# Kernel optimization log

Hardware: AMD Instinct MI355X
Metric: run time of the kernel (lower is better)

The kernel has to match this reference:

```python
import jax, jax.numpy as jnp
import numpy as np

L = 3          # layers
D = 256        # hidden_dim
H = 4          # heads
F = 1024       # ffn_size
IMG = (64, 32) # img_dim
S = IMG[0] * IMG[1]
DK = D // H    # key/query head dim
V = 2 * D      # double_v_dim value dim
DV = V // H    # value head dim
B = 2


def _rel_pos():
    # rotary angles, repeated pairwise as in get_rel_pos
    angle = 1.0 / (10000.0 ** jnp.linspace(0.0, 1.0, DK // 2))
    angle = jnp.repeat(angle, 2)                                  # [DK]
    idx = jnp.arange(S, dtype=jnp.float32)
    sin = jnp.sin(idx[:, None] * angle[None, :])                  # [S, DK]
    cos = jnp.cos(idx[:, None] * angle[None, :])
    # per-head causal decay mask, row-normalized by sqrt(rowsum)
    decay = jnp.log(1.0 - 2.0 ** (-5.0 - jnp.arange(H, dtype=jnp.float32)))  # [H]
    diff = idx[:, None] - idx[None, :]                            # [S, S]
    mask = jnp.where(diff >= 0, jnp.exp(diff[None, :, :] * decay[:, None, None]), 0.0)
    mask = mask / jnp.sqrt(mask.sum(-1, keepdims=True))           # [H, S, S]
    return sin, cos, mask


def _theta_shift(x, sin, cos):
    # x: [B, H, S, DK]; rotate-every-two rotary embedding
    x1, x2 = x[..., ::2], x[..., 1::2]
    rot = jnp.stack([-x2, x1], axis=-1).reshape(x.shape)
    return x * cos + rot * sin


def _ln(x, w, b, eps=1e-5):
    mu = x.mean(-1, keepdims=True)
    var = ((x - mu) ** 2).mean(-1, keepdims=True)
    return (x - mu) / jnp.sqrt(var + eps) * w + b


def _retention(x, sin, cos, mask, Wq, Wk, Wv, Wg, Wo):
    b, s, _ = x.shape
    q = (x @ Wq).reshape(b, s, H, DK).transpose(0, 2, 1, 3)
    k = (x @ Wk).reshape(b, s, H, DK).transpose(0, 2, 1, 3) * (DK ** -0.5)
    v = (x @ Wv).reshape(b, s, H, DV).transpose(0, 2, 1, 3)
    g = x @ Wg                                                    # [b, s, V]
    qr = _theta_shift(q, sin, cos)
    kr = _theta_shift(k, sin, cos)
    qk = jnp.einsum('bhsd,bhtd->bhst', qr, kr) * mask[None]
    denom = jnp.clip(jnp.abs(qk).sum(-1, keepdims=True), 1.0, None)
    qk = qk / jax.lax.stop_gradient(denom)
    o = jnp.einsum('bhst,bhtv->bhsv', qk, v)                      # [b, H, s, DV]
    o = o * jax.lax.rsqrt((o ** 2).mean(-1, keepdims=True) + 1e-6)  # per-head RMSNorm
    o = o.transpose(0, 2, 1, 3).reshape(b, s, V)
    o = (g * jax.nn.sigmoid(g)) * o                               # swish gate
    return o @ Wo


def setup_inputs():
    key = jax.random.key(0)
    ks = jax.random.split(key, 16)
    sc = 0.02
    return {
        'x': jax.random.normal(ks[0], (B, S, D), jnp.float32),
        'Wq': jax.random.normal(ks[1], (L, D, D), jnp.float32) * sc,
        'Wk': jax.random.normal(ks[2], (L, D, D), jnp.float32) * sc,
        'Wv': jax.random.normal(ks[3], (L, D, V), jnp.float32) * sc,
        'Wg': jax.random.normal(ks[4], (L, D, V), jnp.float32) * sc,
        'Wo': jax.random.normal(ks[5], (L, V, D), jnp.float32) * sc,
        'ln1_w': jnp.ones((L, D), jnp.float32),
        'ln1_b': jnp.zeros((L, D), jnp.float32),
        'ln2_w': jnp.ones((L, D), jnp.float32),
        'ln2_b': jnp.zeros((L, D), jnp.float32),
        'W1': jax.random.normal(ks[6], (L, D, F), jnp.float32) * sc,
        'b1': jnp.zeros((L, F), jnp.float32),
        'W2': jax.random.normal(ks[7], (L, F, D), jnp.float32) * sc,
        'b2': jnp.zeros((L, D), jnp.float32),
    }


def reference(x, Wq, Wk, Wv, Wg, Wo, ln1_w, ln1_b, ln2_w, ln2_b, W1, b1, W2, b2):
    sin, cos, mask = _rel_pos()
    for i in range(L):
        y = _retention(_ln(x, ln1_w[i], ln1_b[i]), sin, cos, mask,
                       Wq[i], Wk[i], Wv[i], Wg[i], Wo[i]) + x
        h = _ln(y, ln2_w[i], ln2_b[i])
        x = (jax.nn.gelu(h @ W1[i] + b1[i], approximate=False) @ W2[i] + b2[i]) + y
    return x.reshape(x.shape[0], IMG[0], IMG[1], D)
```

## Files before the change

### kernel.cpp

```cpp
#include <hip/hip_runtime.h>
#include <hip/hip_bf16.h>
#include <cstddef>
#include <cmath>
#include <algorithm>

#define SEQ 2048
#define DMODEL 256
#define NHEAD 4
#define DK 64
#define VDIM 512
#define DV 128
#define NB 2
#define FDIM 1024
#define NROWS (NB*SEQ)
#define QKVGN 1536
#define NSLOT 288

typedef unsigned short u16;
typedef __attribute__((ext_vector_type(8))) short short8;
typedef __attribute__((ext_vector_type(4))) short short4v;
typedef __attribute__((ext_vector_type(4))) float f32x4;

static __device__ __forceinline__ u16 f2b(float f) {
    union { float f; unsigned u; } c; c.f = f;
    unsigned r = c.u + 0x7fffu + ((c.u >> 16) & 1u);
    return (u16)(r >> 16);
}
static __device__ __forceinline__ float b2f(u16 u) {
    union { unsigned u; float f; } c; c.u = ((unsigned)u) << 16; return c.f;
}

static __device__ __forceinline__ f32x4 mfma16_bf16(short4v a, short4v b, f32x4 c) {
    return __builtin_amdgcn_mfma_f32_16x16x16bf16_1k(a, b, c, 0, 0, 0);
}

static __device__ __forceinline__ short4v pack_bf16x4(float a0, float a1, float a2, float a3) {
    union { short4v v; unsigned u[2]; } z;
    union { __hip_bfloat162 h; unsigned u; } p0, p1;
    p0.h = __float22bfloat162_rn(make_float2(a0, a1));
    p1.h = __float22bfloat162_rn(make_float2(a2, a3));
    z.u[0] = p0.u; z.u[1] = p1.u;
    return z.v;
}

#define GLOAD_LDS16(GP, LP) \
    __builtin_amdgcn_global_load_lds((const __attribute__((address_space(1))) void*)(GP), \
                                     (__attribute__((address_space(3))) void*)(LP), 16, 0, 0)

__global__ void tables_kernel(float* __restrict__ sint, float* __restrict__ cost)
{
    int idx = blockIdx.x * 256 + threadIdx.x;
    if (idx >= SEQ * DK) return;
    int s = idx >> 6, d = idx & 63;
    int j = d >> 1;
    float a = powf(10000.f, -(float)j / 31.f);
    float arg = (float)s * a;
    sint[idx] = sinf(arg);
    cost[idx] = cosf(arg);
}

__global__ __launch_bounds__(256) void wconv_kernel(const float* __restrict__ in,
                                                    u16* __restrict__ out, int K, int N,
                                                    size_t in_lstride, size_t out_lstride)
{
    __shared__ float tile[32][33];
    int n0 = blockIdx.x * 32, k0 = blockIdx.y * 32;
    const float* inz = in + (size_t)blockIdx.z * in_lstride;
    u16* outz = out + (size_t)blockIdx.z * out_lstride;
    int tx = threadIdx.x, ty = threadIdx.y;
    #pragma unroll
    for (int r = 0; r < 4; ++r) {
        int kr = ty + r * 8;
        tile[kr][tx] = inz[(size_t)(k0 + kr) * N + n0 + tx];
    }
    __syncthreads();
    #pragma unroll
    for (int r = 0; r < 4; ++r) {
        int nr = ty + r * 8;
        outz[(size_t)(n0 + nr) * K + k0 + tx] = f2b(tile[tx][nr]);
    }
}

__global__ __launch_bounds__(256) void ln_kernel(const float* __restrict__ x,
                                                 const float* __restrict__ w,
                                                 const float* __restrict__ b,
                                                 u16* __restrict__ o)
{
    int row = blockIdx.x;
    int t = threadIdx.x;
    float v = x[(size_t)row * DMODEL + t];
    __shared__ float red[256];
    red[t] = v; __syncthreads();
    for (int st = 128; st > 0; st >>= 1) { if (t < st) red[t] += red[t + st]; __syncthreads(); }
    float mu = red[0] * (1.f / DMODEL);
    __syncthreads();
    red[t] = v * v; __syncthreads();
    for (int st = 128; st > 0; st >>= 1) { if (t < st) red[t] += red[t + st]; __syncthreads(); }
    float var = red[0] * (1.f / DMODEL) - mu * mu;
    o[(size_t)row * DMODEL + t] = f2b((v - mu) * rsqrtf(var + 1e-5f) * w[t] + b[t]);
}

template<int NPART, int HASBIAS>
__global__ __launch_bounds__(256) void lncomb_kernel(const u16* __restrict__ pW,
                                                     const float* __restrict__ bias,
                                                     const float* __restrict__ res,
                                                     const float* __restrict__ w,
                                                     const float* __restrict__ b,
                                                     float* __restrict__ yout,
                                                     u16* __restrict__ o)
{
    int row = blockIdx.x;
    int t = threadIdx.x;
    size_t i = (size_t)row * DMODEL + t;
    const size_t PS = (size_t)NROWS * DMODEL;
    float v = res[i];
    #pragma unroll
    for (int k = 0; k < NPART; ++k) v += b2f(pW[i + k * PS]);
    if (HASBIAS) v += bias[t];
    yout[i] = v;
    __shared__ float red[256];
    red[t] = v; __syncthreads();
    for (int st = 128; st > 0; st >>= 1) { if (t < st) red[t] += red[t + st]; __syncthreads(); }
    float mu = red[0] * (1.f / DMODEL);
    __syncthreads();
    red[t] = v * v; __syncthreads();
    for (int st = 128; st > 0; st >>= 1) { if (t < st) red[t] += red[t + st]; __syncthreads(); }
    float var = red[0] * (1.f / DMODEL) - mu * mu;
    o[i] = f2b((v - mu) * rsqrtf(var + 1e-5f) * w[t] + b[t]);
}

__global__ __launch_bounds__(256) void comb4_kernel(const u16* __restrict__ pW,
                                                    const float* __restrict__ bias,
                                                    const float* __restrict__ yb,
                                                    float* __restrict__ out)
{
    int row = blockIdx.x;
    int t = threadIdx.x;
    size_t i = (size_t)row * DMODEL + t;
    const size_t PS = (size_t)NROWS * DMODEL;
    out[i] = b2f(pW[i]) + b2f(pW[i + PS]) + b2f(pW[i + 2 * PS]) + b2f(pW[i + 3 * PS]) + bias[t] + yb[i];
}

template<int BIAS, int GELU, int ROT, int OUTBF, int SPLIT, int VT>
__global__ __launch_bounds__(256) void gemm64(const u16* __restrict__ A,
                                              const u16* __restrict__ Bt,
                                              void* __restrict__ Cout,
                                              const float* __restrict__ bias,
                                              const float* __restrict__ sint,
                                              const float* __restrict__ cost,
                                              u16* __restrict__ vtout,
                                              int M, int N, int K, int kslice)
{
    __shared__ __align__(16) u16 As[64 * 64];
    __shared__ __align__(16) u16 Bs[64 * 64];
    int bx = blockIdx.x, by = blockIdx.y;
    int tid = threadIdx.x;
    int wave = tid >> 6, lane = tid & 63;
    int wm = wave & 1, wn = wave >> 1;
    int l15 = lane & 15, lg = lane >> 4;
    int kb0 = SPLIT ? blockIdx.z * kslice : 0;
    int kcnt = SPLIT ? kslice : K;

    int L0 = wave * 64 + lane;
    int r0 = L0 >> 3, c0g = (L0 & 7) ^ ((r0 >> 1) & 7);
    int L1 = 256 + wave * 64 + lane;
    int r1 = L1 >> 3, c1g = (L1 & 7) ^ ((r1 >> 1) & 7);
    const u16* Ag0 = A + (size_t)(by * 64 + r0) * K + kb0 + c0g * 8;
    const u16* Ag1 = A + (size_t)(by * 64 + r1) * K + kb0 + c1g * 8;
    const u16* Bg0 = Bt + (size_t)(bx * 64 + r0) * K + kb0 + c0g * 8;
    const u16* Bg1 = Bt + (size_t)(bx * 64 + r1) * K + kb0 + c1g * 8;
    u16* Asw0 = &As[wave * 512];
    u16* Asw1 = &As[2048 + wave * 512];
    u16* Bsw0 = &Bs[wave * 512];
    u16* Bsw1 = &Bs[2048 + wave * 512];

    f32x4 acc[2][2] = {};
    for (int k0 = 0; k0 < kcnt; k0 += 64) {
        GLOAD_LDS16(Ag0 + k0, Asw0);
        GLOAD_LDS16(Ag1 + k0, Asw1);
        GLOAD_LDS16(Bg0 + k0, Bsw0);
        GLOAD_LDS16(Bg1 + k0, Bsw1);
        __syncthreads();
        #pragma unroll
        for (int kk = 0; kk < 2; ++kk) {
            short8 af[2], bf[2];
            #pragma unroll
            for (int i = 0; i < 2; ++i) {
                int ra = wm * 32 + i * 16 + l15;
                int rb = wn * 32 + i * 16 + l15;
                af[i] = *(const short8*)&As[ra * 64 + ((kk * 4 + lg) ^ ((ra >> 1) & 7)) * 8];
                bf[i] = *(const short8*)&Bs[rb * 64 + ((kk * 4 + lg) ^ ((rb >> 1) & 7)) * 8];
            }
            #pragma unroll
            for (int mi = 0; mi < 2; ++mi)
                #pragma unroll
                for (int ni = 0; ni < 2; ++ni)
                    acc[mi][ni] = __builtin_amdgcn_mfma_f32_16x16x32_bf16(af[mi], bf[ni], acc[mi][ni], 0, 0, 0);
        }
        __syncthreads();
    }

    float* Cf = (float*)Cout;
    u16* Ch = (u16*)Cout;
    u16* Chs = (u16*)Cout;
    #pragma unroll
    for (int mi = 0; mi < 2; ++mi)
        #pragma unroll
        for (int ni = 0; ni < 2; ++ni) {
            int colb = bx * 64 + wn * 32 + ni * 16;
            if (VT && colb >= 512 && colb < 1024) {
                int col = colb + l15;
                int z = ((by >> 5) << 2) + ((col - 512) >> 7);
                int dv = (col - 512) & 127;
                int s0b = (by * 64 + wm * 32) & (SEQ - 1);
                short4v pk = pack_bf16x4(acc[mi][ni][0], acc[mi][ni][1], acc[mi][ni][2], acc[mi][ni][3]);
                *(short4v*)(vtout + (size_t)(z * DV + dv) * SEQ + s0b + lg * 8 + mi * 4) = pk;
            } else {
                #pragma unroll
                for (int r = 0; r < 4; ++r) {
                    int row = by * 64 + wm * 32 + mi * 16 + lg * 4 + r;
                    int col = colb + l15;
                    float v = acc[mi][ni][r];
                    if (ROT) {
                        float pv = __shfl_xor(v, 1);
                        if (col < 512) {
                            int s = row & (SEQ - 1);
                            int dk = col & 63;
                            float c = cost[(s << 6) + dk], sn = sint[(s << 6) + dk];
                            float rv = (col & 1) ? (v * c + pv * sn) : (v * c - pv * sn);
                            v = (col < 256) ? rv : rv * 0.125f;
                        }
                    }
                    if (BIAS) v += bias[col];
                    if (GELU) v = 0.5f * v * (1.f + erff(v * 0.70710678118654752f));
                    if (SPLIT)      Chs[(size_t)blockIdx.z * M * N + (size_t)row * N + col] = f2b(v);
                    else if (OUTBF) Ch[(size_t)row * N + col] = f2b(v);
                    else            Cf[(size_t)row * N + col] = v;
                }
            }
        }
}

__global__ __launch_bounds__(256) void retention_p1(
    const u16* __restrict__ qkvg, const u16* __restrict__ vt,
    u16* __restrict__ po, float* __restrict__ pden)
{
    __shared__ __align__(16) u16 Klds[2][2048];
    __shared__ __align__(16) u16 Vlds[2][4096];

    int bid = blockIdx.x;
    int bh = bid & 7;
    int f = bid >> 3;
    int a = 0, base = 0;
    while (f >= base + 8 * (a + 1)) { base += 8 * (a + 1); ++a; }
    int segs = f - base;
    int qt = 8 * a + segs / (a + 1);
    int ch = segs % (a + 1);
    int b = bh >> 2, h = bh & 3;
    int slot = bh * NSLOT + f;

    int tid = threadIdx.x;
    int wave = tid >> 6, lane = tid & 63;
    int wq = wave >> 1, wv = wave & 1;
    int l15 = lane & 15, lg = lane >> 4;

    float rgeo = 1.f - exp2f(-5.f - (float)h);
    float dec2 = log2f(rgeo);
    float step = exp2f(dec2 * -32.f);

    const u16* qbase  = qkvg + (size_t)b * SEQ * QKVGN + h * 64;
    const u16* kbase  = qbase + 256;
    const u16* vtg    = vt + (size_t)bh * DV * SEQ;

    int q0w = qt * 32 + wq * 16;
    short8 qf0 = *(const short8*)(qbase + (size_t)(q0w + l15) * QKVGN + lg * 8);
    short8 qf1 = *(const short8*)(qbase + (size_t)(q0w + l15) * QKVGN + 32 + lg * 8);

    int tb = ch * 8;
    int t_last = (ch == a) ? qt : (tb + 7);
    int hasdiag = (ch == a);

    float rinv  = exp2f(-dec2);
    float r16   = exp2f(dec2 * -16.f);
    float et00 = exp2f(dec2 * -(float)(tb * 32 + lg * 4));
    float et01 = et00 * rinv;
    float et02 = et01 * rinv;
    float et03 = et02 * rinv;
    float et10 = et00 * r16, et11 = et01 * r16, et12 = et02 * r16, et13 = et03 * r16;

    f32x4 oacc0 = {0.f,0.f,0.f,0.f}, oacc1 = {0.f,0.f,0.f,0.f};
    f32x4 oacc2 = {0.f,0.f,0.f,0.f}, oacc3 = {0.f,0.f,0.f,0.f};
    float den_l = 0.f;

#define STAGE(BUF, TI) do { \
    int t0_ = (TI) * 32; \
    _Pragma("unroll") \
    for (int ii = 0; ii < 3; ++ii) { \
        int inst_ = wave * 3 + ii; \
        if (inst_ < 4) { \
            const u16* g_ = kbase + (size_t)(t0_ + (lane & 31)) * QKVGN + (2 * inst_ + (lane >> 5)) * 8; \
            GLOAD_LDS16(g_, &Klds[BUF][inst_ * 512]); \
        } else { \
            int j_ = inst_ - 4; \
            const u16* g_ = vtg + (size_t)(j_ * 16 + (lane >> 2)) * SEQ + t0_ + (lane & 3) * 8; \
            GLOAD_LDS16(g_, &Vlds[BUF][j_ * 512]); \
        } \
    } \
} while (0)

#define BODY(BUF, DIAG) do { \
    const u16* kb_ = &Klds[BUF][0]; \
    const u16* vb_ = &Vlds[BUF][0]; \
    short8 k00 = *(const short8*)(kb_ + (lg    ) * 256 + l15 * 8); \
    short8 k01 = *(const short8*)(kb_ + (4 + lg) * 256 + l15 * 8); \
    short8 k10 = *(const short8*)(kb_ + (lg    ) * 256 + (16 + l15) * 8); \
    short8 k11 = *(const short8*)(kb_ + (4 + lg) * 256 + (16 + l15) * 8); \
    short8 V0 = *(const short8*)(vb_ + (wv * 64 +      l15) * 32 + lg * 8); \
    short8 V1 = *(const short8*)(vb_ + (wv * 64 + 16 + l15) * 32 + lg * 8); \
    short8 V2 = *(const short8*)(vb_ + (wv * 64 + 32 + l15) * 32 + lg * 8); \
    short8 V3 = *(const short8*)(vb_ + (wv * 64 + 48 + l15) * 32 + lg * 8); \
    f32x4 s0 = {0.f,0.f,0.f,0.f}, s1 = {0.f,0.f,0.f,0.f}; \
    s0 = __builtin_amdgcn_mfma_f32_16x16x32_bf16(k00, qf0, s0, 0, 0, 0); \
    s0 = __builtin_amdgcn_mfma_f32_16x16x32_bf16(k01, qf1, s0, 0, 0, 0); \
    s1 = __builtin_amdgcn_mfma_f32_16x16x32_bf16(k10, qf0, s1, 0, 0, 0); \
    s1 = __builtin_amdgcn_mfma_f32_16x16x32_bf16(k11, qf1, s1, 0, 0, 0); \
    float a0 = s0[0] * et00, a1 = s0[1] * et01, a2 = s0[2] * et02, a3 = s0[3] * et03; \
    float c0 = s1[0] * et10, c1 = s1[1] * et11, c2 = s1[2] * et12, c3 = s1[3] * et13; \
    if (DIAG) { \
        int qr_ = wq * 16 + l15, t0r_ = lg * 4; \
        a0 = (t0r_ +  0 <= qr_) ? a0 : 0.f;  a1 = (t0r_ +  1 <= qr_) ? a1 : 0.f; \
        a2 = (t0r_ +  2 <= qr_) ? a2 : 0.f;  a3 = (t0r_ +  3 <= qr_) ? a3 : 0.f; \
        c0 = (t0r_ + 16 <= qr_) ? c0 : 0.f;  c1 = (t0r_ + 17 <= qr_) ? c1 : 0.f; \
        c2 = (t0r_ + 18 <= qr_) ? c2 : 0.f;  c3 = (t0r_ + 19 <= qr_) ? c3 : 0.f; \
    } \
    den_l += fabsf(a0) + fabsf(a1) + fabsf(a2) + fabsf(a3) \
           + fabsf(c0) + fabsf(c1) + fabsf(c2) + fabsf(c3); \
    short4v pa0 = pack_bf16x4(a0, a1, a2, a3); \
    short4v pa1 = pack_bf16x4(c0, c1, c2, c3); \
    oacc0 = mfma16_bf16(pa0, __builtin_shufflevector(V0, V0, 0, 1, 2, 3), oacc0); \
    oacc1 = mfma16_bf16(pa0, __builtin_shufflevector(V1, V1, 0, 1, 2, 3), oacc1); \
    oacc2 = mfma16_bf16(pa0, __builtin_shufflevector(V2, V2, 0, 1, 2, 3), oacc2); \
    oacc3 = mfma16_bf16(pa0, __builtin_shufflevector(V3, V3, 0, 1, 2, 3), oacc3); \
    oacc0 = mfma16_bf16(pa1, __builtin_shufflevector(V0, V0, 4, 5, 6, 7), oacc0); \
    oacc1 = mfma16_bf16(pa1, __builtin_shufflevector(V1, V1, 4, 5, 6, 7), oacc1); \
    oacc2 = mfma16_bf16(pa1, __builtin_shufflevector(V2, V2, 4, 5, 6, 7), oacc2); \
    oacc3 = mfma16_bf16(pa1, __builtin_shufflevector(V3, V3, 4, 5, 6, 7), oacc3); \
    et00 *= step; et01 *= step; et02 *= step; et03 *= step; \
    et10 *= step; et11 *= step; et12 *= step; et13 *= step; \
} while (0)

    int ti = tb;
    STAGE(0, tb);
    __syncthreads();
    for (; ti + 2 <= t_last; ti += 2) {
        STAGE(1, ti + 1);
        BODY(0, 0);
        __syncthreads();
        STAGE(0, ti + 2);
        BODY(1, 0);
        __syncthreads();
    }
    if (ti < t_last) {
        STAGE(1, ti + 1);
        BODY(0, 0);
        __syncthreads();
        BODY(1, hasdiag);
    } else {
        BODY(0, hasdiag);
    }
#undef STAGE
#undef BODY

    den_l += __shfl_xor(den_l, 16);
    den_l += __shfl_xor(den_l, 32);
    if (lane < 16)
        pden[(size_t)slot * 32 + wq * 16 + l15] = den_l;

    u16* pobase = po + (size_t)slot * (32 * 128) + (wq * 16 + lg * 4) * 128 + wv * 64 + l15;
    #pragma unroll
    for (int r = 0; r < 4; ++r) {
        pobase[r * 128 +  0] = f2b(oacc0[r]);
        pobase[r * 128 + 16] = f2b(oacc1[r]);
        pobase[r * 128 + 32] = f2b(oacc2[r]);
        pobase[r * 128 + 48] = f2b(oacc3[r]);
    }
}

__global__ __launch_bounds__(256) void retention_p2(
    const u16* __restrict__ po, const float* __restrict__ pden,
    const u16* __restrict__ qkvg, u16* __restrict__ og)
{
    int bid = blockIdx.x;
    int bh = bid & 7;
    int qt = bid >> 3;
    int b = bh >> 2, h = bh & 3;
    int aa = qt >> 3;
    int sbase = bh * NSLOT + 4 * aa * (aa + 1) + (qt & 7) * (aa + 1);
    int nch = aa + 1;
    int t = threadIdx.x;
    int row = t >> 3, c0 = (t & 7) * 16;
    int q = qt * 32 + row;

    float den = 0.f;
    for (int k = 0; k < nch; ++k) den += pden[(size_t)(sbase + k) * 32 + row];
    float acc[16];
    #pragma unroll
    for (int j = 0; j < 16; ++j) acc[j] = 0.f;
    for (int k = 0; k < nch; ++k) {
        const u16* p = po + (size_t)(sbase + k) * (32 * 128) + row * 128 + c0;
        #pragma unroll
        for (int j = 0; j < 16; ++j) acc[j] += b2f(p[j]);
    }
    float rgeo = 1.f - exp2f(-5.f - (float)h);
    float dec2 = log2f(rgeo);
    float rp1 = exp2f(dec2 * (float)(q + 1));
    float cs = (1.f - rp1) / (1.f - rgeo);
    float invs = rsqrtf(cs);
    float eqv = exp2f(dec2 * (float)q);
    float d = fmaxf(den * eqv * invs, 1.f);
    float scl = eqv * invs / d;
    float ss = 0.f;
    #pragma unroll
    for (int j = 0; j < 16; ++j) { float v = acc[j] * scl; acc[j] = v; ss += v * v; }
    ss += __shfl_xor(ss, 1); ss += __shfl_xor(ss, 2); ss += __shfl_xor(ss, 4);
    float rms = rsqrtf(ss * (1.f / DV) + 1e-6f);

    const u16* gbase = qkvg + ((size_t)(b * SEQ + q)) * QKVGN + 1024 + h * DV + c0;
    u16* obase = og + ((size_t)(b * SEQ + q)) * VDIM + h * DV + c0;
    #pragma unroll
    for (int j = 0; j < 16; ++j) {
        float gv = b2f(gbase[j]);
        float sig = 1.f / (1.f + __expf(-gv));
        obase[j] = f2b(gv * sig * acc[j] * rms);
    }
}

extern "C" void kernel_launch(void* const* d_in, const int* in_sizes, int n_in,
                              void* d_out, int out_size, void* d_ws, size_t ws_size,
                              hipStream_t stream)
{
    const float* x0    = (const float*)d_in[0];
    const float* Wq    = (const float*)d_in[1];
    const float* Wk    = (const float*)d_in[2];
    const float* Wv    = (const float*)d_in[3];
    const float* Wg    = (const float*)d_in[4];
    const float* Wo    = (const float*)d_in[5];
    const float* ln1w  = (const float*)d_in[6];
    const float* ln1b  = (const float*)d_in[7];
    const float* ln2w  = (const float*)d_in[8];
    const float* ln2b  = (const float*)d_in[9];
    const float* W1    = (const float*)d_in[10];
    const float* b1    = (const float*)d_in[11];
    const float* W2    = (const float*)d_in[12];
    const float* b2    = (const float*)d_in[13];

    char* ws = (char*)d_ws;
    size_t off = 0;
    auto alloc = [&](size_t bytes) { char* p = ws + off; off += (bytes + 255) & ~(size_t)255; return p; };

    float* sin_t = (float*)alloc(SEQ * DK * 4);
    float* cos_t = (float*)alloc(SEQ * DK * 4);
    u16* wqkvg_t = (u16*)alloc((size_t)3 * QKVGN * DMODEL * 2);
    u16* wo_t    = (u16*)alloc((size_t)3 * DMODEL * VDIM * 2);
    u16* w1_t    = (u16*)alloc((size_t)3 * FDIM * DMODEL * 2);
    u16* w2_t    = (u16*)alloc((size_t)3 * DMODEL * FDIM * 2);
    u16* qkvg    = (u16*)alloc((size_t)NROWS * QKVGN * 2);
    u16* xln     = (u16*)alloc((size_t)NROWS * DMODEL * 2);
    u16* vt      = (u16*)alloc((size_t)NB * NHEAD * DV * SEQ * 2);
    float* yb    = (float*)alloc((size_t)NROWS * DMODEL * 4);
    float* xbuf  = (float*)alloc((size_t)NROWS * DMODEL * 4);
    u16* po      = (u16*)alloc((size_t)8 * NSLOT * 32 * 128 * 2);
    float* pden  = (float*)alloc((size_t)8 * NSLOT * 32 * 4);
    u16* ff1 = qkvg;
    u16* h2  = xln;
    u16* ogb = vt;
    u16* pWh = po;

    tables_kernel<<<(SEQ * DK + 255) / 256, 256, 0, stream>>>(sin_t, cos_t);
    dim3 tb(32, 8);
    const size_t WLQ = (size_t)QKVGN * DMODEL;
    wconv_kernel<<<dim3(8, 8, 3),  tb, 0, stream>>>(Wq, wqkvg_t,              DMODEL, DMODEL, (size_t)DMODEL*DMODEL, WLQ);
    wconv_kernel<<<dim3(8, 8, 3),  tb, 0, stream>>>(Wk, wqkvg_t + 256 * 256,  DMODEL, DMODEL, (size_t)DMODEL*DMODEL, WLQ);
    wconv_kernel<<<dim3(16, 8, 3), tb, 0, stream>>>(Wv, wqkvg_t + 512 * 256,  DMODEL, VDIM,   (size_t)DMODEL*VDIM,   WLQ);
    wconv_kernel<<<dim3(16, 8, 3), tb, 0, stream>>>(Wg, wqkvg_t + 1024 * 256, DMODEL, VDIM,   (size_t)DMODEL*VDIM,   WLQ);
    wconv_kernel<<<dim3(8, 16, 3), tb, 0, stream>>>(Wo, wo_t, VDIM,   DMODEL, (size_t)VDIM*DMODEL,   (size_t)VDIM*DMODEL);
    wconv_kernel<<<dim3(32, 8, 3), tb, 0, stream>>>(W1, w1_t, DMODEL, FDIM,   (size_t)DMODEL*FDIM,   (size_t)DMODEL*FDIM);
    wconv_kernel<<<dim3(8, 32, 3), tb, 0, stream>>>(W2, w2_t, FDIM,   DMODEL, (size_t)FDIM*DMODEL,   (size_t)FDIM*DMODEL);

    ln_kernel<<<NROWS, 256, 0, stream>>>(x0, ln1w, ln1b, xln);

    const float* xres = x0;
    for (int i = 0; i < 3; ++i) {
        const u16* wqkvgi = wqkvg_t + (size_t)i * QKVGN * DMODEL;
        const u16* woi = wo_t + (size_t)i * DMODEL * VDIM;
        const u16* w1i = w1_t + (size_t)i * FDIM * DMODEL;
        const u16* w2i = w2_t + (size_t)i * DMODEL * FDIM;

        gemm64<0,0,1,1,0,1><<<dim3(QKVGN/64, NROWS/64), 256, 0, stream>>>(
            xln, wqkvgi, qkvg, nullptr, sin_t, cos_t, vt, NROWS, QKVGN, DMODEL, 0);

        retention_p1<<<dim3(NSLOT * NB * NHEAD), 256, 0, stream>>>(qkvg, vt, po, pden);
        retention_p2<<<dim3((SEQ/32) * NB * NHEAD), 256, 0, stream>>>(po, pden, qkvg, ogb);

        gemm64<0,0,0,0,1,0><<<dim3(DMODEL/64, NROWS/64, 4), 256, 0, stream>>>(
            ogb, woi, pWh, nullptr, nullptr, nullptr, nullptr, NROWS, DMODEL, VDIM, 128);
        lncomb_kernel<4,0><<<NROWS, 256, 0, stream>>>(pWh, nullptr, xres,
            ln2w + i * DMODEL, ln2b + i * DMODEL, yb, h2);

        gemm64<1,1,0,1,0,0><<<dim3(FDIM/64, NROWS/64), 256, 0, stream>>>(
            h2, w1i, ff1, b1 + (size_t)i * FDIM, nullptr, nullptr, nullptr, NROWS, FDIM, DMODEL, 0);

        gemm64<0,0,0,0,1,0><<<dim3(DMODEL/64, NROWS/64, 4), 256, 0, stream>>>(
            ff1, w2i, pWh, nullptr, nullptr, nullptr, nullptr, NROWS, DMODEL, FDIM, 256);

        if (i < 2) {
            lncomb_kernel<4,1><<<NROWS, 256, 0, stream>>>(pWh, b2 + (size_t)i * DMODEL, yb,
                ln1w + (i + 1) * DMODEL, ln1b + (i + 1) * DMODEL, xbuf, xln);
            xres = xbuf;
        } else {
            comb4_kernel<<<NROWS, 256, 0, stream>>>(pWh, b2 + (size_t)i * DMODEL, yb, (float*)d_out);
        }
    }
}
```

Baseline: 281.8 us.

## Widen retention query tile to 64 rows with each wave covering all value columns

The chunked retention kernel now processes 64 query rows per block instead of 32. Each of the four waves owns 16 query rows and accumulates all 128 value columns, where before two waves split the value dimension. Each staged K/V tile is therefore reused by twice as many queries, which halves the K/V global-to-LDS traffic and the partial-result slot count. The causal mask now uses global positions so the last two key tiles can be masked. The cost is twice as many accumulator registers per wave, half as many blocks, and a combine kernel reworked to 64-row tiles with 32 columns per thread.

```diff
diff --git a/kernel.cpp b/kernel.cpp
--- a/kernel.cpp
+++ b/kernel.cpp
@@ -14,7 +14,7 @@
 #define FDIM 1024
 #define NROWS (NB*SEQ)
 #define QKVGN 1536
-#define NSLOT 288
+#define NSLOT 144
 
 typedef unsigned short u16;
 typedef __attribute__((ext_vector_type(8))) short short8;
@@ -252,16 +252,16 @@
     int bh = bid & 7;
     int f = bid >> 3;
     int a = 0, base = 0;
-    while (f >= base + 8 * (a + 1)) { base += 8 * (a + 1); ++a; }
+    while (f >= base + 4 * (a + 1)) { base += 4 * (a + 1); ++a; }
     int segs = f - base;
-    int qt = 8 * a + segs / (a + 1);
+    int qt64 = 4 * a + segs / (a + 1);
     int ch = segs % (a + 1);
     int b = bh >> 2, h = bh & 3;
     int slot = bh * NSLOT + f;
 
     int tid = threadIdx.x;
     int wave = tid >> 6, lane = tid & 63;
-    int wq = wave >> 1, wv = wave & 1;
+    int wq = wave;
     int l15 = lane & 15, lg = lane >> 4;
 
     float rgeo = 1.f - exp2f(-5.f - (float)h);
@@ -272,12 +272,12 @@
     const u16* kbase  = qbase + 256;
     const u16* vtg    = vt + (size_t)bh * DV * SEQ;
 
-    int q0w = qt * 32 + wq * 16;
+    int q0w = qt64 * 64 + wq * 16;
     short8 qf0 = *(const short8*)(qbase + (size_t)(q0w + l15) * QKVGN + lg * 8);
     short8 qf1 = *(const short8*)(qbase + (size_t)(q0w + l15) * QKVGN + 32 + lg * 8);
 
     int tb = ch * 8;
-    int t_last = (ch == a) ? qt : (tb + 7);
+    int t_last = (ch == a) ? (2 * qt64 + 1) : (tb + 7);
     int hasdiag = (ch == a);
 
     float rinv  = exp2f(-dec2);
@@ -290,6 +290,8 @@
 
     f32x4 oacc0 = {0.f,0.f,0.f,0.f}, oacc1 = {0.f,0.f,0.f,0.f};
     f32x4 oacc2 = {0.f,0.f,0.f,0.f}, oacc3 = {0.f,0.f,0.f,0.f};
+    f32x4 oacc4 = {0.f,0.f,0.f,0.f}, oacc5 = {0.f,0.f,0.f,0.f};
+    f32x4 oacc6 = {0.f,0.f,0.f,0.f}, oacc7 = {0.f,0.f,0.f,0.f};
     float den_l = 0.f;
 
 #define STAGE(BUF, TI) do { \
@@ -308,17 +310,32 @@
     } \
 } while (0)
 
-#define BODY(BUF, DIAG) do { \
+#define PVSTEP(PA, SEL0, SEL1, SEL2, SEL3, SEL4, SEL5, SEL6, SEL7) do { \
+    oacc0 = mfma16_bf16(PA, __builtin_shufflevector(V0, V0, SEL0, SEL1, SEL2, SEL3), oacc0); \
+    oacc1 = mfma16_bf16(PA, __builtin_shufflevector(V1, V1, SEL0, SEL1, SEL2, SEL3), oacc1); \
+    oacc2 = mfma16_bf16(PA, __builtin_shufflevector(V2, V2, SEL0, SEL1, SEL2, SEL3), oacc2); \
+    oacc3 = mfma16_bf16(PA, __builtin_shufflevector(V3, V3, SEL0, SEL1, SEL2, SEL3), oacc3); \
+    oacc4 = mfma16_bf16(PA, __builtin_shufflevector(V4, V4, SEL0, SEL1, SEL2, SEL3), oacc4); \
+    oacc5 = mfma16_bf16(PA, __builtin_shufflevector(V5, V5, SEL0, SEL1, SEL2, SEL3), oacc5); \
+    oacc6 = mfma16_bf16(PA, __builtin_shufflevector(V6, V6, SEL0, SEL1, SEL2, SEL3), oacc6); \
+    oacc7 = mfma16_bf16(PA, __builtin_shufflevector(V7, V7, SEL0, SEL1, SEL2, SEL3), oacc7); \
+} while (0)
+
+#define BODY(BUF, T0, DIAG) do { \
     const u16* kb_ = &Klds[BUF][0]; \
     const u16* vb_ = &Vlds[BUF][0]; \
     short8 k00 = *(const short8*)(kb_ + (lg    ) * 256 + l15 * 8); \
     short8 k01 = *(const short8*)(kb_ + (4 + lg) * 256 + l15 * 8); \
     short8 k10 = *(const short8*)(kb_ + (lg    ) * 256 + (16 + l15) * 8); \
     short8 k11 = *(const short8*)(kb_ + (4 + lg) * 256 + (16 + l15) * 8); \
-    short8 V0 = *(const short8*)(vb_ + (wv * 64 +      l15) * 32 + lg * 8); \
-    short8 V1 = *(const short8*)(vb_ + (wv * 64 + 16 + l15) * 32 + lg * 8); \
-    short8 V2 = *(const short8*)(vb_ + (wv * 64 + 32 + l15) * 32 + lg * 8); \
-    short8 V3 = *(const short8*)(vb_ + (wv * 64 + 48 + l15) * 32 + lg * 8); \
+    short8 V0 = *(const short8*)(vb_ + (      l15) * 32 + lg * 8); \
+    short8 V1 = *(const short8*)(vb_ + (16 +  l15) * 32 + lg * 8); \
+    short8 V2 = *(const short8*)(vb_ + (32 +  l15) * 32 + lg * 8); \
+    short8 V3 = *(const short8*)(vb_ + (48 +  l15) * 32 + lg * 8); \
+    short8 V4 = *(const short8*)(vb_ + (64 +  l15) * 32 + lg * 8); \
+    short8 V5 = *(const short8*)(vb_ + (80 +  l15) * 32 + lg * 8); \
+    short8 V6 = *(const short8*)(vb_ + (96 +  l15) * 32 + lg * 8); \
+    short8 V7 = *(const short8*)(vb_ + (112 + l15) * 32 + lg * 8); \
     f32x4 s0 = {0.f,0.f,0.f,0.f}, s1 = {0.f,0.f,0.f,0.f}; \
     s0 = __builtin_amdgcn_mfma_f32_16x16x32_bf16(k00, qf0, s0, 0, 0, 0); \
     s0 = __builtin_amdgcn_mfma_f32_16x16x32_bf16(k01, qf1, s0, 0, 0, 0); \
@@ -327,24 +344,19 @@
     float a0 = s0[0] * et00, a1 = s0[1] * et01, a2 = s0[2] * et02, a3 = s0[3] * et03; \
     float c0 = s1[0] * et10, c1 = s1[1] * et11, c2 = s1[2] * et12, c3 = s1[3] * et13; \
     if (DIAG) { \
-        int qr_ = wq * 16 + l15, t0r_ = lg * 4; \
-        a0 = (t0r_ +  0 <= qr_) ? a0 : 0.f;  a1 = (t0r_ +  1 <= qr_) ? a1 : 0.f; \
-        a2 = (t0r_ +  2 <= qr_) ? a2 : 0.f;  a3 = (t0r_ +  3 <= qr_) ? a3 : 0.f; \
-        c0 = (t0r_ + 16 <= qr_) ? c0 : 0.f;  c1 = (t0r_ + 17 <= qr_) ? c1 : 0.f; \
-        c2 = (t0r_ + 18 <= qr_) ? c2 : 0.f;  c3 = (t0r_ + 19 <= qr_) ? c3 : 0.f; \
+        int qr_ = q0w + l15; \
+        int tg_ = (T0) + lg * 4; \
+        a0 = (tg_ +  0 <= qr_) ? a0 : 0.f;  a1 = (tg_ +  1 <= qr_) ? a1 : 0.f; \
+        a2 = (tg_ +  2 <= qr_) ? a2 : 0.f;  a3 = (tg_ +  3 <= qr_) ? a3 : 0.f; \
+        c0 = (tg_ + 16 <= qr_) ? c0 : 0.f;  c1 = (tg_ + 17 <= qr_) ? c1 : 0.f; \
+        c2 = (tg_ + 18 <= qr_) ? c2 : 0.f;  c3 = (tg_ + 19 <= qr_) ? c3 : 0.f; \
     } \
     den_l += fabsf(a0) + fabsf(a1) + fabsf(a2) + fabsf(a3) \
            + fabsf(c0) + fabsf(c1) + fabsf(c2) + fabsf(c3); \
     short4v pa0 = pack_bf16x4(a0, a1, a2, a3); \
     short4v pa1 = pack_bf16x4(c0, c1, c2, c3); \
-    oacc0 = mfma16_bf16(pa0, __builtin_shufflevector(V0, V0, 0, 1, 2, 3), oacc0); \
-    oacc1 = mfma16_bf16(pa0, __builtin_shufflevector(V1, V1, 0, 1, 2, 3), oacc1); \
-    oacc2 = mfma16_bf16(pa0, __builtin_shufflevector(V2, V2, 0, 1, 2, 3), oacc2); \
-    oacc3 = mfma16_bf16(pa0, __builtin_shufflevector(V3, V3, 0, 1, 2, 3), oacc3); \
-    oacc0 = mfma16_bf16(pa1, __builtin_shufflevector(V0, V0, 4, 5, 6, 7), oacc0); \
-    oacc1 = mfma16_bf16(pa1, __builtin_shufflevector(V1, V1, 4, 5, 6, 7), oacc1); \
-    oacc2 = mfma16_bf16(pa1, __builtin_shufflevector(V2, V2, 4, 5, 6, 7), oacc2); \
-    oacc3 = mfma16_bf16(pa1, __builtin_shufflevector(V3, V3, 4, 5, 6, 7), oacc3); \
+    PVSTEP(pa0, 0, 1, 2, 3, 0, 0, 0, 0); \
+    PVSTEP(pa1, 4, 5, 6, 7, 0, 0, 0, 0); \
     et00 *= step; et01 *= step; et02 *= step; et03 *= step; \
     et10 *= step; et11 *= step; et12 *= step; et13 *= step; \
 } while (0)
@@ -354,35 +366,40 @@
     __syncthreads();
     for (; ti + 2 <= t_last; ti += 2) {
         STAGE(1, ti + 1);
-        BODY(0, 0);
+        BODY(0, ti * 32, 0);
         __syncthreads();
         STAGE(0, ti + 2);
-        BODY(1, 0);
+        BODY(1, (ti + 1) * 32, 0);
         __syncthreads();
     }
     if (ti < t_last) {
         STAGE(1, ti + 1);
-        BODY(0, 0);
+        BODY(0, ti * 32, hasdiag);
         __syncthreads();
-        BODY(1, hasdiag);
+        BODY(1, (ti + 1) * 32, hasdiag);
     } else {
-        BODY(0, hasdiag);
+        BODY(0, ti * 32, hasdiag);
     }
 #undef STAGE
+#undef PVSTEP
 #undef BODY
 
     den_l += __shfl_xor(den_l, 16);
     den_l += __shfl_xor(den_l, 32);
     if (lane < 16)
-        pden[(size_t)slot * 32 + wq * 16 + l15] = den_l;
-
-    u16* pobase = po + (size_t)slot * (32 * 128) + (wq * 16 + lg * 4) * 128 + wv * 64 + l15;
+        pden[(size_t)slot * 64 + wq * 16 + l15] = den_l;
+
+    u16* pobase = po + (size_t)slot * (64 * 128) + (wq * 16 + lg * 4) * 128 + l15;
     #pragma unroll
     for (int r = 0; r < 4; ++r) {
-        pobase[r * 128 +  0] = f2b(oacc0[r]);
-        pobase[r * 128 + 16] = f2b(oacc1[r]);
-        pobase[r * 128 + 32] = f2b(oacc2[r]);
-        pobase[r * 128 + 48] = f2b(oacc3[r]);
+        pobase[r * 128 +   0] = f2b(oacc0[r]);
+        pobase[r * 128 +  16] = f2b(oacc1[r]);
+        pobase[r * 128 +  32] = f2b(oacc2[r]);
+        pobase[r * 128 +  48] = f2b(oacc3[r]);
+        pobase[r * 128 +  64] = f2b(oacc4[r]);
+        pobase[r * 128 +  80] = f2b(oacc5[r]);
+        pobase[r * 128 +  96] = f2b(oacc6[r]);
+        pobase[r * 128 + 112] = f2b(oacc7[r]);
     }
 }
 
@@ -392,24 +409,24 @@
 {
     int bid = blockIdx.x;
     int bh = bid & 7;
-    int qt = bid >> 3;
+    int qt64 = bid >> 3;
     int b = bh >> 2, h = bh & 3;
-    int aa = qt >> 3;
-    int sbase = bh * NSLOT + 4 * aa * (aa + 1) + (qt & 7) * (aa + 1);
+    int aa = qt64 >> 2, rr = qt64 & 3;
+    int sbase = bh * NSLOT + qt64 + 2 * aa * (aa - 1) + rr * aa;
     int nch = aa + 1;
     int t = threadIdx.x;
-    int row = t >> 3, c0 = (t & 7) * 16;
-    int q = qt * 32 + row;
+    int row = t >> 2, c0 = (t & 3) * 32;
+    int q = qt64 * 64 + row;
 
     float den = 0.f;
-    for (int k = 0; k < nch; ++k) den += pden[(size_t)(sbase + k) * 32 + row];
-    float acc[16];
-    #pragma unroll
-    for (int j = 0; j < 16; ++j) acc[j] = 0.f;
+    for (int k = 0; k < nch; ++k) den += pden[(size_t)(sbase + k) * 64 + row];
+    float acc[32];
+    #pragma unroll
+    for (int j = 0; j < 32; ++j) acc[j] = 0.f;
     for (int k = 0; k < nch; ++k) {
-        const u16* p = po + (size_t)(sbase + k) * (32 * 128) + row * 128 + c0;
+        const u16* p = po + (size_t)(sbase + k) * (64 * 128) + row * 128 + c0;
         #pragma unroll
-        for (int j = 0; j < 16; ++j) acc[j] += b2f(p[j]);
+        for (int j = 0; j < 32; ++j) acc[j] += b2f(p[j]);
     }
     float rgeo = 1.f - exp2f(-5.f - (float)h);
     float dec2 = log2f(rgeo);
@@ -421,14 +438,14 @@
     float scl = eqv * invs / d;
     float ss = 0.f;
     #pragma unroll
-    for (int j = 0; j < 16; ++j) { float v = acc[j] * scl; acc[j] = v; ss += v * v; }
-    ss += __shfl_xor(ss, 1); ss += __shfl_xor(ss, 2); ss += __shfl_xor(ss, 4);
+    for (int j = 0; j < 32; ++j) { float v = acc[j] * scl; acc[j] = v; ss += v * v; }
+    ss += __shfl_xor(ss, 1); ss += __shfl_xor(ss, 2);
     float rms = rsqrtf(ss * (1.f / DV) + 1e-6f);
 
     const u16* gbase = qkvg + ((size_t)(b * SEQ + q)) * QKVGN + 1024 + h * DV + c0;
     u16* obase = og + ((size_t)(b * SEQ + q)) * VDIM + h * DV + c0;
     #pragma unroll
-    for (int j = 0; j < 16; ++j) {
+    for (int j = 0; j < 32; ++j) {
         float gv = b2f(gbase[j]);
         float sig = 1.f / (1.f + __expf(-gv));
         obase[j] = f2b(gv * sig * acc[j] * rms);
@@ -469,8 +486,8 @@
     u16* vt      = (u16*)alloc((size_t)NB * NHEAD * DV * SEQ * 2);
     float* yb    = (float*)alloc((size_t)NROWS * DMODEL * 4);
     float* xbuf  = (float*)alloc((size_t)NROWS * DMODEL * 4);
-    u16* po      = (u16*)alloc((size_t)8 * NSLOT * 32 * 128 * 2);
-    float* pden  = (float*)alloc((size_t)8 * NSLOT * 32 * 4);
+    u16* po      = (u16*)alloc((size_t)8 * NSLOT * 64 * 128 * 2);
+    float* pden  = (float*)alloc((size_t)8 * NSLOT * 64 * 4);
     u16* ff1 = qkvg;
     u16* h2  = xln;
     u16* ogb = vt;
@@ -500,7 +517,7 @@
             xln, wqkvgi, qkvg, nullptr, sin_t, cos_t, vt, NROWS, QKVGN, DMODEL, 0);
 
         retention_p1<<<dim3(NSLOT * NB * NHEAD), 256, 0, stream>>>(qkvg, vt, po, pden);
-        retention_p2<<<dim3((SEQ/32) * NB * NHEAD), 256, 0, stream>>>(po, pden, qkvg, ogb);
+        retention_p2<<<dim3((SEQ/64) * NB * NHEAD), 256, 0, stream>>>(po, pden, qkvg, ogb);
 
         gemm64<0,0,0,0,1,0><<<dim3(DMODEL/64, NROWS/64, 4), 256, 0, stream>>>(
             ogb, woi, pWh, nullptr, nullptr, nullptr, nullptr, NROWS, DMODEL, VDIM, 128);
```

After: 276.0 us. 2.0% less time.
